# Kernel tuning notes

Hardware: AMD Instinct MI355X
Metric: run time of the kernel (lower is better)

The kernel has to match this reference:

```python
import math
import jax, jax.numpy as jnp
import numpy as np
from jax.scipy.linalg import cho_factor, cho_solve, block_diag

NUM_SENSORS = 64
T_STEPS = 2048
LOG2PI = float(np.log(2.0 * np.pi))

NCV_PROCESS_NOISE = np.array([[1.0/3.0, 0.0, 0.5, 0.0],
                              [0.0, 1.0/3.0, 0.0, 0.5],
                              [0.5, 0.0, 1.0, 0.0],
                              [0.0, 0.5, 0.0, 1.0]], dtype=np.float32)
NCV_TRANSITION_MATRIX = np.array([[1.0, 0.0, 1.0, 0.0],
                                  [0.0, 1.0, 0.0, 1.0],
                                  [0.0, 0.0, 1.0, 0.0],
                                  [0.0, 0.0, 0.0, 1.0]], dtype=np.float32)


def setup_inputs() -> dict:
    key = jax.random.key(0)
    k1, k2 = jax.random.split(key)
    track = jax.random.normal(k1, (T_STEPS, 2), dtype=jnp.float32)
    # positive covariance scales for the bias prior (torch param init ~ ones)
    bias_scales = jax.random.uniform(k2, (2,), jnp.float32, 0.5, 1.5)
    obs_noise = jnp.float32(0.7)
    trans_noise = jnp.float32(0.3)
    return {"track": track, "bias_scales": bias_scales,
            "obs_noise": obs_noise, "trans_noise": trans_noise}


def _hmm_forward(track, bias_scales, obs_noise, trans_noise, num_sensors):
    S = num_sensors
    OD = 2 * S           # obs_dim
    D = OD + 4           # augmented latent: [bias(OD); state(4)]
    T = track.shape[0]
    dt = track.dtype

    # observation matrix exactly as in torch source:
    # eye(4,2).expand(S,4,2).transpose(0,-1).reshape(4, OD)
    E = jnp.eye(4, 2, dtype=dt)
    Hobs = jnp.transpose(jnp.broadcast_to(E, (S, 4, 2)), (2, 1, 0)).reshape(4, OD)
    # augmented emission: y = bias + state @ Hobs  ->  H_aug z
    Haug = jnp.concatenate([jnp.eye(OD, dtype=dt), Hobs.T], axis=1)  # (OD, D)

    F = jnp.asarray(NCV_TRANSITION_MATRIX, dt)
    # trans scale_tril = trans_noise * chol(NCV_Q) -> cov = trans_noise^2 * NCV_Q
    Qs = (trans_noise ** 2) * jnp.asarray(NCV_PROCESS_NOISE, dt)
    A = block_diag(jnp.eye(OD, dtype=dt), F)                         # (D, D)
    Q = block_diag(jnp.zeros((OD, OD), dt), Qs)                      # (D, D)
    # obs scale_tril = obs_noise * I -> cov = obs_noise^2 * I
    R = (obs_noise ** 2) * jnp.eye(OD, dtype=dt)

    # bias prior covariance = diag(bias_scales interleaved per sensor)
    bias_var = jnp.broadcast_to(bias_scales, (S, 2)).reshape(-1)     # (OD,)
    m0 = jnp.zeros((D,), dt)
    P0 = jnp.diag(jnp.concatenate([bias_var, jnp.ones((4,), dt)]))

    # obs vector per step: x.expand(S,2).reshape(-1) (interleaved repeat)
    ys = jnp.broadcast_to(track[:, None, :], (T, S, 2)).reshape(T, OD)

    def step(carry, y):
        m, P, ll = carry
        # predict
        mp = A @ m
        Pp = A @ P @ A.T + Q
        # innovation
        HP = Haug @ Pp                      # (OD, D)
        Sm = HP @ Haug.T + R                # (OD, OD)
        cf = cho_factor(Sm, lower=True)
        v = y - Haug @ mp                   # (OD,)
        # update
        K = cho_solve(cf, HP)               # S^{-1} H Pp, (OD, D)
        m_new = mp + K.T @ v
        P_new = Pp - HP.T @ K
        P_new = 0.5 * (P_new + P_new.T)
        # log-likelihood of innovation
        logdet = 2.0 * jnp.sum(jnp.log(jnp.diag(cf[0])))
        quad = v @ cho_solve(cf, v)
        ll = ll - 0.5 * (OD * LOG2PI + logdet + quad)
        return (m_new, P_new, ll), None

    (mT, PT, ll), _ = jax.lax.scan(step, (m0, P0, jnp.zeros((), dt)), ys)
    # funsor's remaining Gaussian over (bias, state_T) has precision = inv(filtered cov)
    cfP = cho_factor(PT, lower=True)
    prec = cho_solve(cfP, jnp.eye(D, dtype=dt))
    return ll, prec


def reference(track, bias_scales, obs_noise, trans_noise):
    return _hmm_forward(track, bias_scales, obs_noise, trans_noise, NUM_SENSORS)
```

## Files before the change

### kernel.cpp

```cpp
#include <hip/hip_runtime.h>
#include <math.h>

#define L2PI 1.8378770664093454835606594728112
#define LN2  0.69314718055994530941723212145818

struct LP {
    float jFF, jFL, jFB, jLL, jLB, jBB;
    float hF, hL, hB, g, dm, de;
};

struct Cn { float qa, qb, qc, wa, wb, ri, Cstep; };

__device__ __forceinline__ float shf(float v, int s) { return __shfl(v, s, 64); }
__device__ __forceinline__ float sx (float v, int m) { return __shfl_xor(v, m, 64); }

#define LGKM0() do { \
    asm volatile("s_waitcnt lgkmcnt(0)" ::: "memory"); \
    __builtin_amdgcn_sched_barrier(0); \
} while (0)

#define OFF_S   0
#define OFF_F1  16
#define OFF_F2T 32
#define OFF_MT  48
#define OFF_HM  64
#define GSTRIDE 152

#define WSR_OFF 8192

__device__ __forceinline__ float4 ld4(const float* p) {
    return *(const float4*)p;
}
__device__ __forceinline__ float dot4(float4 a, float4 b) {
    float s = a.x * b.x;
    s = fmaf(a.y, b.y, s);
    s = fmaf(a.z, b.z, s);
    s = fmaf(a.w, b.w, s);
    return s;
}
__device__ __forceinline__ float sel4(float x0, float x1, float x2, float x3, int k) {
    return (k == 0) ? x0 : ((k == 1) ? x1 : ((k == 2) ? x2 : x3));
}

struct Adj4 { float e[4][4]; };
__device__ __forceinline__ Adj4 adj4(const float4& Ra, const float4& Rb,
                                     const float4& Rc, const float4& Rd) {
    float sS[4][4];
    sS[0][0]=Ra.x; sS[0][1]=Ra.y; sS[0][2]=Ra.z; sS[0][3]=Ra.w;
    sS[1][0]=Rb.x; sS[1][1]=Rb.y; sS[1][2]=Rb.z; sS[1][3]=Rb.w;
    sS[2][0]=Rc.x; sS[2][1]=Rc.y; sS[2][2]=Rc.z; sS[2][3]=Rc.w;
    sS[3][0]=Rd.x; sS[3][1]=Rd.y; sS[3][2]=Rd.z; sS[3][3]=Rd.w;
    Adj4 A;
    #pragma unroll
    for (int a = 0; a < 4; ++a) {
        const int c0 = (a == 0) ? 1 : 0;
        const int c1 = (a <= 1) ? 2 : 1;
        const int c2 = (a <= 2) ? 3 : 2;
        #pragma unroll
        for (int b = 0; b < 4; ++b) {
            const int r0 = (b == 0) ? 1 : 0;
            const int r1 = (b <= 1) ? 2 : 1;
            const int r2 = (b <= 2) ? 3 : 2;
            float m00 = sS[r0][c0], m01 = sS[r0][c1], m02 = sS[r0][c2];
            float m10 = sS[r1][c0], m11 = sS[r1][c1], m12 = sS[r1][c2];
            float m20 = sS[r2][c0], m21 = sS[r2][c1], m22 = sS[r2][c2];
            float d0 = fmaf(m11, m22, -m12*m21);
            float d1 = fmaf(m10, m22, -m12*m20);
            float d2 = fmaf(m10, m21, -m11*m20);
            float det3 = m00*d0 - m01*d1 + m02*d2;
            A.e[a][b] = (((a + b) & 1) ? -det3 : det3);
        }
    }
    return A;
}
__device__ __forceinline__ float det4_colj(const Adj4& A, const float4& RJ, int j) {
    float a0j = sel4(A.e[0][0], A.e[0][1], A.e[0][2], A.e[0][3], j);
    float a1j = sel4(A.e[1][0], A.e[1][1], A.e[1][2], A.e[1][3], j);
    float a2j = sel4(A.e[2][0], A.e[2][1], A.e[2][2], A.e[2][3], j);
    float a3j = sel4(A.e[3][0], A.e[3][1], A.e[3][2], A.e[3][3], j);
    float t0 = RJ.x * a0j, t1 = RJ.y * a1j, t2 = RJ.z * a2j, t3 = RJ.w * a3j;
    return (t0 + t1) + (t2 + t3);
}

__device__ __forceinline__ LP init_lane(float x0, float x1, const Cn& C, int i, int j) {
    LP P;
    float v = 0.0f;
    if (i == j) v = (i < 2) ? C.qa : C.qc;
    if ((i ^ j) == 2) v = C.wa;
    P.jFF = v;
    v = 0.0f;
    if (j == (i & 1))     v = (i < 2) ? -C.qa : -C.wa;
    if (j == (i & 1) + 2) v = (i < 2) ? -C.qb : -C.wb;
    P.jFL = v;
    P.jFB = 0.0f;
    v = 0.0f;
    if (i == j) v = ((i < 2) ? C.qa : C.qc) + (((i & 1) == 0) ? 2.0f*C.ri : 0.0f);
    if ((i ^ j) == 2) v = C.qb;
    P.jLL = v;
    P.jLB = (((i == 0) && (j < 2)) || ((i == 2) && (j >= 2))) ? C.ri : 0.0f;
    P.jBB = (i == j) ? C.ri : 0.0f;
    P.hF = 0.0f;
    P.hL = ((j & 1) == 0) ? C.ri * (x0 + x1) : 0.0f;
    P.hB = C.ri * ((j & 1) ? x1 : x0);
    P.g  = -C.ri * (x0*x0 + x1*x1) + C.Cstep;
    P.dm = 1.0f; P.de = 0.0f;
    return P;
}

__device__ __forceinline__ LP compose(const LP& P1, const LP& P2, float* gl, int i, int j) {
    float hm = P1.hL + P2.hF;
    float Mb = P1.jLB + P2.jFB;
    float S  = P1.jLL + P2.jFF;
    float dm = P1.dm * P2.dm;
    float de = P1.de + P2.de;
    { int ex; dm = frexpf(dm, &ex); de += (float)ex; }
    const int ij = 4*i + j, ji = 4*j + i;

    gl[OFF_S   + ij] = S;
    gl[OFF_F1  + ij] = P1.jFL;
    gl[OFF_F2T + ji] = P2.jFL;
    gl[OFF_MT  + ji] = Mb;
    if (i == 0) gl[OFF_HM + j] = hm;
    LGKM0();
    float4 Ra = ld4(gl + OFF_S + 0);
    float4 Rb = ld4(gl + OFF_S + 4);
    float4 Rc = ld4(gl + OFF_S + 8);
    float4 Rd = ld4(gl + OFF_S + 12);
    float4 RJ = ld4(gl + OFF_S + 4*j);
    float4 f1r4 = ld4(gl + OFF_F1  + 4*i);
    float4 f1T4 = ld4(gl + OFF_F1  + 4*j);
    float4 f2c4 = ld4(gl + OFF_F2T + 4*j);
    float4 f2T4 = ld4(gl + OFF_F2T + 4*i);
    float4 mc4  = ld4(gl + OFF_MT  + 4*j);
    float4 mT4  = ld4(gl + OFF_MT  + 4*i);
    float4 hm4  = ld4(gl + OFF_HM);

    Adj4 A = adj4(Ra, Rb, Rc, Rd);
    float det = det4_colj(A, RJ, j);
    dm *= det; { int ex; dm = frexpf(dm, &ex); de += (float)ex; }
    const float rdet = 1.0f / det;
    float4 sie0 = make_float4(A.e[0][0]*rdet, A.e[0][1]*rdet, A.e[0][2]*rdet, A.e[0][3]*rdet);
    float4 sie1 = make_float4(A.e[1][0]*rdet, A.e[1][1]*rdet, A.e[1][2]*rdet, A.e[1][3]*rdet);
    float4 sie2 = make_float4(A.e[2][0]*rdet, A.e[2][1]*rdet, A.e[2][2]*rdet, A.e[2][3]*rdet);
    float4 sie3 = make_float4(A.e[3][0]*rdet, A.e[3][1]*rdet, A.e[3][2]*rdet, A.e[3][3]*rdet);

    float4 a1r4 = make_float4(dot4(f1r4, sie0), dot4(f1r4, sie1),
                              dot4(f1r4, sie2), dot4(f1r4, sie3));
    float4 a1j4 = make_float4(dot4(f1T4, sie0), dot4(f1T4, sie1),
                              dot4(f1T4, sie2), dot4(f1T4, sie3));
    float4 c1c4 = make_float4(dot4(sie0, mc4), dot4(sie1, mc4),
                              dot4(sie2, mc4), dot4(sie3, mc4));
    float4 b2c4 = make_float4(dot4(sie0, f2c4), dot4(sie1, f2c4),
                              dot4(sie2, f2c4), dot4(sie3, f2c4));
    float4 v44  = make_float4(dot4(sie0, hm4), dot4(sie1, hm4),
                              dot4(sie2, hm4), dot4(sie3, hm4));

    LP R;
    R.jFF = P1.jFF - dot4(a1r4, f1T4);
    R.jFL = -dot4(a1r4, f2c4);
    R.jFB = P1.jFB - dot4(a1r4, mc4);
    R.jLL = P2.jLL - dot4(f2T4, b2c4);
    R.jLB = P2.jLB - dot4(f2T4, c1c4);
    R.jBB = P1.jBB + P2.jBB - dot4(mT4, c1c4);
    R.hF  = P1.hF - dot4(a1j4, hm4);
    R.hL  = P2.hL - dot4(f2c4, v44);
    R.hB  = P1.hB + P2.hB - dot4(mc4, v44);
    R.g   = P1.g + P2.g + 2.0f*(float)L2PI + 0.5f*dot4(hm4, v44);
    R.dm = dm; R.de = de;
    return R;
}

__device__ __forceinline__ LP fetchx(const LP& P, int m) {
    LP O;
    O.jFF = sx(P.jFF,m); O.jFL = sx(P.jFL,m); O.jFB = sx(P.jFB,m);
    O.jLL = sx(P.jLL,m); O.jLB = sx(P.jLB,m); O.jBB = sx(P.jBB,m);
    O.hF  = sx(P.hF,m);  O.hL  = sx(P.hL,m);  O.hB  = sx(P.hB,m);
    O.g   = sx(P.g,m);   O.dm  = sx(P.dm,m);  O.de  = sx(P.de,m);
    return O;
}
__device__ __forceinline__ LP csel(bool up, const LP& O, const LP& P) {
    LP A;
    A.jFF = up?O.jFF:P.jFF; A.jFL = up?O.jFL:P.jFL; A.jFB = up?O.jFB:P.jFB;
    A.jLL = up?O.jLL:P.jLL; A.jLB = up?O.jLB:P.jLB; A.jBB = up?O.jBB:P.jBB;
    A.hF  = up?O.hF :P.hF;  A.hL  = up?O.hL :P.hL;  A.hB  = up?O.hB :P.hB;
    A.g   = up?O.g  :P.g;   A.dm  = up?O.dm :P.dm;  A.de  = up?O.de :P.de;
    return A;
}
__device__ __forceinline__ void pot_store(float* p, const LP& P) {
    p[0]=P.jFF; p[1]=P.jFL; p[2]=P.jFB; p[3]=P.jLL; p[4]=P.jLB; p[5]=P.jBB;
    p[6]=P.hF;  p[7]=P.hL;  p[8]=P.hB;  p[9]=P.g;   p[10]=P.dm; p[11]=P.de;
}
__device__ __forceinline__ LP pot_load(const float* p) {
    LP P;
    P.jFF=p[0]; P.jFL=p[1]; P.jFB=p[2]; P.jLL=p[3]; P.jLB=p[4]; P.jBB=p[5];
    P.hF=p[6];  P.hL=p[7];  P.hB=p[8];  P.g=p[9];   P.dm=p[10]; P.de=p[11];
    return P;
}
__device__ __forceinline__ void pot_store4(float* p, const LP& P) {
    *(float4*)(p + 0) = make_float4(P.jFF, P.jFL, P.jFB, P.jLL);
    *(float4*)(p + 4) = make_float4(P.jLB, P.jBB, P.hF,  P.hL);
    *(float4*)(p + 8) = make_float4(P.hB,  P.g,   P.dm,  P.de);
}
__device__ __forceinline__ LP pot_load4(const float* p) {
    float4 a = ld4(p + 0), b = ld4(p + 4), c = ld4(p + 8);
    LP P;
    P.jFF=a.x; P.jFL=a.y; P.jFB=a.z; P.jLL=a.w;
    P.jLB=b.x; P.jBB=b.y; P.hF=b.z;  P.hL=b.w;
    P.hB=c.x;  P.g=c.y;   P.dm=c.z;  P.de=c.w;
    return P;
}

__global__ __launch_bounds__(512)
void hmm_produce(const float* __restrict__ track,
                 const float* __restrict__ obs_noise_p,
                 const float* __restrict__ trans_noise_p,
                 float* __restrict__ ws)
{
    __shared__ float pool[2][8][16][13];
    __shared__ __align__(16) float cbuf[32 * GSTRIDE];
    const int tid = (int)threadIdx.x;
    const int l = tid & 63, w = tid >> 6;
    const int i = (l >> 2) & 3, j = l & 3, g = (l >> 4) & 3;
    const int gid = w * 4 + g;
    float* gl = &cbuf[(size_t)gid * GSTRIDE];
    const int bid = (int)blockIdx.x;

    const double sg2d = (double)obs_noise_p[0] * (double)obs_noise_p[0];
    const double qn2d = (double)trans_noise_p[0] * (double)trans_noise_p[0];

    Cn C;
    C.qa = (float)(12.0/qn2d); C.qb = (float)(-6.0/qn2d); C.qc = (float)(4.0/qn2d);
    C.wa = (float)(6.0/qn2d);  C.wb = (float)(-2.0/qn2d);
    C.ri = (float)(32.0/sg2d);
    C.Cstep = (float)(-2.0*log(2.0*M_PI*sg2d/32.0) - 2.0*L2PI
                      - 0.5*(4.0*log(qn2d) - 2.0*log(12.0)));

    const int t0 = (bid * 32 + gid) * 2;
    LP P;
    #pragma unroll 1
    for (int op = 0; op < 6; ++op) {
        LP A, Bp;
        if (op == 0) {
            A  = init_lane(track[2*t0+0], track[2*t0+1], C, i, j);
            Bp = init_lane(track[2*t0+2], track[2*t0+3], C, i, j);
        } else if (op < 3) {
            const int m = 16 << (op - 1);
            LP O = fetchx(P, m);
            const bool up = (l & m) != 0;
            A  = csel(up, O, P);
            Bp = csel(up, P, O);
        } else {
            const int s = 1 << (op - 3);
            const int buf = (op - 3) & 1;
            if (l < 16) pot_store(&pool[buf][w][l][0], P);
            __syncthreads();
            LP O = pot_load(&pool[buf][w ^ s][l & 15][0]);
            const bool up = (w & s) != 0;
            A  = csel(up, O, P);
            Bp = csel(up, P, O);
        }
        P = compose(A, Bp, gl, i, j);
    }
    if (w == 0 && l < 16)
        pot_store4(ws + ((size_t)bid * 16 + l) * 12, P);
}

__global__ __launch_bounds__(512)
void hmm_tree(const float* __restrict__ bias_scales,
              const float* __restrict__ obs_noise_p,
              float* __restrict__ ws)
{
    __shared__ float pool[2][8][16][13];
    __shared__ __align__(16) float cbuf[32 * GSTRIDE];
    const int tid = (int)threadIdx.x;
    const int l = tid & 63, w = tid >> 6;
    const int i = (l >> 2) & 3, j = l & 3, g = (l >> 4) & 3;
    const int gid = w * 4 + g;
    float* gl = &cbuf[(size_t)gid * GSTRIDE];
    float* wsr = ws + WSR_OFF;

    const double sg2d = (double)obs_noise_p[0] * (double)obs_noise_p[0];
    const double a00 = (double)bias_scales[0];
    const double a01 = (double)bias_scales[1];
    const double Td = 2048.0;
    const double c0d = sg2d/a00, c1d = sg2d/a01;
    const double llconst = -31.0*(Td*(L2PI + log(sg2d)) + log((c0d+Td)/c0d))
                           -31.0*(Td*(L2PI + log(sg2d)) + log((c1d+Td)/c1d))
                           -2.0*Td*log(32.0);
    const float gconst = (float)(-4.0*L2PI + 2.0*log(32.0) - log(a00) - log(a01));

    LP P = pot_load4(ws + ((size_t)gid * 16 + (l & 15)) * 12);
    #pragma unroll 1
    for (int op = 0; op < 5; ++op) {
        LP A, Bp;
        if (op < 2) {
            const int m = 16 << op;
            LP O = fetchx(P, m);
            const bool up = (l & m) != 0;
            A  = csel(up, O, P);
            Bp = csel(up, P, O);
        } else {
            const int s = 1 << (op - 2);
            const int buf = (op - 2) & 1;
            if (l < 16) pot_store(&pool[buf][w][l][0], P);
            __syncthreads();
            LP O = pot_load(&pool[buf][w ^ s][l & 15][0]);
            const bool up = (w & s) != 0;
            A  = csel(up, O, P);
            Bp = csel(up, P, O);
        }
        P = compose(A, Bp, gl, i, j);
    }

    if (w == 0) {
        const float a0i = (float)((i & 1) ? a01 : a00);
        P.jFF += (i == j) ? 1.0f : 0.0f;
        P.jBB += (i == j) ? 32.0f / a0i : 0.0f;
        P.g   += gconst;
        float dm = P.dm, de = P.de;
        const int ij = 4*i + j, ji = 4*j + i;

        gl[OFF_S   + ij] = P.jFF;
        gl[OFF_F1  + ji] = P.jFL;
        gl[OFF_F2T + ji] = P.jFB;
        if (i == 0) gl[OFF_HM + j] = P.hF;
        LGKM0();
        float4 Ra = ld4(gl + OFF_S + 0);
        float4 Rb = ld4(gl + OFF_S + 4);
        float4 Rc = ld4(gl + OFF_S + 8);
        float4 Rd = ld4(gl + OFF_S + 12);
        float4 RJ = ld4(gl + OFF_S + 4*j);
        float4 fr4 = ld4(gl + OFF_F1  + 4*i);
        float4 fT4 = ld4(gl + OFF_F1  + 4*j);
        float4 bc4 = ld4(gl + OFF_F2T + 4*i);
        float4 bT4 = ld4(gl + OFF_F2T + 4*j);
        float4 hf4 = ld4(gl + OFF_HM);

        Adj4 A = adj4(Ra, Rb, Rc, Rd);
        float det = det4_colj(A, RJ, j);
        dm *= det; { int ex; dm = frexpf(dm, &ex); de += (float)ex; }
        const float rdet = 1.0f / det;
        float4 sie0 = make_float4(A.e[0][0]*rdet, A.e[0][1]*rdet, A.e[0][2]*rdet, A.e[0][3]*rdet);
        float4 sie1 = make_float4(A.e[1][0]*rdet, A.e[1][1]*rdet, A.e[1][2]*rdet, A.e[1][3]*rdet);
        float4 sie2 = make_float4(A.e[2][0]*rdet, A.e[2][1]*rdet, A.e[2][2]*rdet, A.e[2][3]*rdet);
        float4 sie3 = make_float4(A.e[3][0]*rdet, A.e[3][1]*rdet, A.e[3][2]*rdet, A.e[3][3]*rdet);

        float4 ylc4 = make_float4(dot4(sie0, fT4), dot4(sie1, fT4),
                                  dot4(sie2, fT4), dot4(sie3, fT4));
        float4 ybc4 = make_float4(dot4(sie0, bT4), dot4(sie1, bT4),
                                  dot4(sie2, bT4), dot4(sie3, bT4));
        float4 yfc4 = make_float4(dot4(sie0, hf4), dot4(sie1, hf4),
                                  dot4(sie2, hf4), dot4(sie3, hf4));
        float s1  = dot4(fr4, ylc4);
        float s2  = dot4(fr4, ybc4);
        float s3  = dot4(bc4, ybc4);
        float sh1 = dot4(fT4, yfc4);
        float sh2 = dot4(bT4, yfc4);
        float qF  = dot4(hf4, yfc4);

        float J8ss = P.jLL - s1;
        float J8sb = P.jLB - s2;
        float J8bb = P.jBB - s3;
        float h8s  = P.hL - sh1;
        float h8b  = P.hB - sh2;
        float g8   = P.g + 2.0f*(float)L2PI + 0.5f*qF;

        const int I = l >> 3, J = l & 7, i4 = I & 3, j4 = J & 3;
        float ss  = shf(J8ss, 4*i4 + j4);
        float sb  = shf(J8sb, 4*i4 + j4);
        float sbT = shf(J8sb, 4*j4 + i4);
        float bb  = shf(J8bb, 4*i4 + j4);
        float A8 = (I < 4) ? ((J < 4) ? ss : sb) : ((J < 4) ? sbT : bb);
        const float J8sav = A8;
        float h8v = (J < 4) ? shf(h8s, j4) : shf(h8b, j4);
        float h8r = (I < 4) ? shf(h8s, i4) : shf(h8b, i4);
        float K8 = (I == J) ? 1.0f : 0.0f;
        #pragma unroll 1
        for (int p = 0; p < 8; ++p) {
            float piv = shf(A8, 9*p);
            dm *= piv; { int ex; dm = frexpf(dm, &ex); de += (float)ex; }
            float ip = 1.0f / piv;
            float Ap = shf(A8, 8*p + J) * ip;
            float Kp = shf(K8, 8*p + J) * ip;
            float f  = shf(A8, 8*I + p);
            bool isp = (I == p);
            A8 = isp ? A8 * ip : fmaf(-f, Ap, A8);
            K8 = isp ? K8 * ip : fmaf(-f, Kp, K8);
        }
        float tq = h8r * K8 * h8v;
        tq += sx(tq,1); tq += sx(tq,2); tq += sx(tq,4);
        tq += sx(tq,8); tq += sx(tq,16); tq += sx(tq,32);

        double ll = (double)g8 + 4.0*L2PI
                    - 0.5*(log((double)dm) + (double)de*LN2) + 0.5*(double)tq;
        ll += llconst;

        const float i32 = 1.0f/32.0f, irn = 0.176776695296637f;
        int a = (I >= 4) ? I - 4 : I + 4;
        int b = (J >= 4) ? J - 4 : J + 4;
        float scale = (I >= 4 && J >= 4) ? i32 : (((I >= 4) != (J >= 4)) ? irn : 1.0f);
        wsr[1 + 8*a + b] = J8sav * scale;
        if (l < 4) {
            double a0k = (l & 1) ? a01 : a00;
            wsr[65 + l] = (float)(a0k*sg2d/(sg2d + Td*a0k));
        }
        if (l == 0) wsr[0] = (float)ll;
    }
}

__global__ __launch_bounds__(256)
void hmm_expand(const float* __restrict__ wsr,
                float* __restrict__ out)
{
    const int idx = (int)blockIdx.x * 256 + (int)threadIdx.x;
    const int total = 1 + 132*132;
    if (idx >= total) return;
    const float inv32 = 1.0f/32.0f;
    const float invrn = 0.176776695296637f;
    float v;
    if (idx == 0) {
        v = wsr[0];
    } else {
        int el = idx - 1;
        int r = el / 132;
        int cc = el - 132*r;
        if (r < 128) {
            int ki = ((r >> 6) << 1) | (r & 1);
            if (cc < 128) {
                int kj = ((cc >> 6) << 1) | (cc & 1);
                v = wsr[1 + 8*ki + kj] * inv32;
                if (ki == kj) {
                    float ia = 1.0f / wsr[65 + ki];
                    v -= ia * inv32;
                    if (r == cc) v += ia;
                }
            } else {
                v = wsr[1 + 8*ki + (cc - 124)] * invrn;
            }
        } else {
            if (cc < 128) {
                int kj = ((cc >> 6) << 1) | (cc & 1);
                v = wsr[1 + 8*kj + (r - 124)] * invrn;
            } else {
                v = wsr[1 + 8*(r - 124) + (cc - 124)];
            }
        }
    }
    out[idx] = v;
}

extern "C" void kernel_launch(void* const* d_in, const int* in_sizes, int n_in,
                              void* d_out, int out_size, void* d_ws, size_t ws_size,
                              hipStream_t stream) {
    (void)in_sizes; (void)n_in; (void)out_size; (void)ws_size;
    const float* track       = (const float*)d_in[0];
    const float* bias_scales = (const float*)d_in[1];
    const float* obs_noise   = (const float*)d_in[2];
    const float* trans_noise = (const float*)d_in[3];
    float* out = (float*)d_out;
    float* ws  = (float*)d_ws;
    hipLaunchKernelGGL(hmm_produce, dim3(32), dim3(512), 0, stream,
                       track, obs_noise, trans_noise, ws);
    hipLaunchKernelGGL(hmm_tree, dim3(1), dim3(512), 0, stream,
                       bias_scales, obs_noise, ws);
    hipLaunchKernelGGL(hmm_expand, dim3(69), dim3(256), 0, stream,
                       (const float*)(ws + WSR_OFF), out);
}
```

Measured before the change: 82.39 us.

## Distribute 4x4 inverse across lanes in tree compose and final reduction

In the tree kernel, the per-lane full adjugate/inverse of the 4x4 Schur block is replaced by each lane computing a single 3x3 cofactor, with the determinant reduced via xor shuffles. The inverse and the intermediate products are then exchanged through LDS (or, in the final step, through cross-lane shuffles) rather than every lane recomputing them redundantly. This reduces per-lane ALU work and register pressure but adds extra LDS round trips, waits and shuffles on a latency-bound serial path. The leaf kernel keeps the original compose.

New measurement: 81.36 us. About the same (-1.3%).

```diff
diff --git a/kernel.cpp b/kernel.cpp
--- a/kernel.cpp
+++ b/kernel.cpp
@@ -19,11 +19,21 @@
     __builtin_amdgcn_sched_barrier(0); \
 } while (0)
 
-#define OFF_S   0
-#define OFF_F1  16
-#define OFF_F2T 32
-#define OFF_MT  48
-#define OFF_HM  64
+#define PO_S   0
+#define PO_F1  16
+#define PO_F2T 32
+#define PO_MT  48
+#define PO_HM  64
+#define TO_S   0
+#define TO_SI  16
+#define TO_F1  32
+#define TO_F2T 48
+#define TO_MT  64
+#define TO_A1  80
+#define TO_C1T 96
+#define TO_B2T 112
+#define TO_V4  128
+#define TO_HM  132
 #define GSTRIDE 152
 
 #define WSR_OFF 8192
@@ -107,7 +117,7 @@
     return P;
 }
 
-__device__ __forceinline__ LP compose(const LP& P1, const LP& P2, float* gl, int i, int j) {
+__device__ __forceinline__ LP compose_li(const LP& P1, const LP& P2, float* gl, int i, int j) {
     float hm = P1.hL + P2.hF;
     float Mb = P1.jLB + P2.jFB;
     float S  = P1.jLL + P2.jFF;
@@ -116,24 +126,24 @@
     { int ex; dm = frexpf(dm, &ex); de += (float)ex; }
     const int ij = 4*i + j, ji = 4*j + i;
 
-    gl[OFF_S   + ij] = S;
-    gl[OFF_F1  + ij] = P1.jFL;
-    gl[OFF_F2T + ji] = P2.jFL;
-    gl[OFF_MT  + ji] = Mb;
-    if (i == 0) gl[OFF_HM + j] = hm;
+    gl[PO_S   + ij] = S;
+    gl[PO_F1  + ij] = P1.jFL;
+    gl[PO_F2T + ji] = P2.jFL;
+    gl[PO_MT  + ji] = Mb;
+    if (i == 0) gl[PO_HM + j] = hm;
     LGKM0();
-    float4 Ra = ld4(gl + OFF_S + 0);
-    float4 Rb = ld4(gl + OFF_S + 4);
-    float4 Rc = ld4(gl + OFF_S + 8);
-    float4 Rd = ld4(gl + OFF_S + 12);
-    float4 RJ = ld4(gl + OFF_S + 4*j);
-    float4 f1r4 = ld4(gl + OFF_F1  + 4*i);
-    float4 f1T4 = ld4(gl + OFF_F1  + 4*j);
-    float4 f2c4 = ld4(gl + OFF_F2T + 4*j);
-    float4 f2T4 = ld4(gl + OFF_F2T + 4*i);
-    float4 mc4  = ld4(gl + OFF_MT  + 4*j);
-    float4 mT4  = ld4(gl + OFF_MT  + 4*i);
-    float4 hm4  = ld4(gl + OFF_HM);
+    float4 Ra = ld4(gl + PO_S + 0);
+    float4 Rb = ld4(gl + PO_S + 4);
+    float4 Rc = ld4(gl + PO_S + 8);
+    float4 Rd = ld4(gl + PO_S + 12);
+    float4 RJ = ld4(gl + PO_S + 4*j);
+    float4 f1r4 = ld4(gl + PO_F1  + 4*i);
+    float4 f1T4 = ld4(gl + PO_F1  + 4*j);
+    float4 f2c4 = ld4(gl + PO_F2T + 4*j);
+    float4 f2T4 = ld4(gl + PO_F2T + 4*i);
+    float4 mc4  = ld4(gl + PO_MT  + 4*j);
+    float4 mT4  = ld4(gl + PO_MT  + 4*i);
+    float4 hm4  = ld4(gl + PO_HM);
 
     Adj4 A = adj4(Ra, Rb, Rc, Rd);
     float det = det4_colj(A, RJ, j);
@@ -154,6 +164,89 @@
                               dot4(sie2, f2c4), dot4(sie3, f2c4));
     float4 v44  = make_float4(dot4(sie0, hm4), dot4(sie1, hm4),
                               dot4(sie2, hm4), dot4(sie3, hm4));
+
+    LP R;
+    R.jFF = P1.jFF - dot4(a1r4, f1T4);
+    R.jFL = -dot4(a1r4, f2c4);
+    R.jFB = P1.jFB - dot4(a1r4, mc4);
+    R.jLL = P2.jLL - dot4(f2T4, b2c4);
+    R.jLB = P2.jLB - dot4(f2T4, c1c4);
+    R.jBB = P1.jBB + P2.jBB - dot4(mT4, c1c4);
+    R.hF  = P1.hF - dot4(a1j4, hm4);
+    R.hL  = P2.hL - dot4(f2c4, v44);
+    R.hB  = P1.hB + P2.hB - dot4(mc4, v44);
+    R.g   = P1.g + P2.g + 2.0f*(float)L2PI + 0.5f*dot4(hm4, v44);
+    R.dm = dm; R.de = de;
+    return R;
+}
+
+__device__ __forceinline__ LP compose_3r(const LP& P1, const LP& P2, float* gl, int i, int j) {
+    float hm = P1.hL + P2.hF;
+    float Mb = P1.jLB + P2.jFB;
+    float S  = P1.jLL + P2.jFF;
+    float dm = P1.dm * P2.dm;
+    float de = P1.de + P2.de;
+    { int ex; dm = frexpf(dm, &ex); de += (float)ex; }
+    const int ij = 4*i + j, ji = 4*j + i;
+
+    gl[TO_S   + ij] = S;
+    gl[TO_F1  + ij] = P1.jFL;
+    gl[TO_F2T + ji] = P2.jFL;
+    gl[TO_MT  + ji] = Mb;
+    if (i == 0) gl[TO_HM + j] = hm;
+    LGKM0();
+
+    const int r0 = (j == 0) ? 1 : 0;
+    const int r1 = (j <= 1) ? 2 : 1;
+    const int r2 = (j <= 2) ? 3 : 2;
+    float4 R0 = ld4(gl + TO_S + 4*r0);
+    float4 R1 = ld4(gl + TO_S + 4*r1);
+    float4 R2 = ld4(gl + TO_S + 4*r2);
+    float4 RJ = ld4(gl + TO_S + 4*j);
+    float4 f1r4 = ld4(gl + TO_F1  + 4*i);
+    float4 f1T4 = ld4(gl + TO_F1  + 4*j);
+    float4 f2c4 = ld4(gl + TO_F2T + 4*j);
+    float4 f2T4 = ld4(gl + TO_F2T + 4*i);
+    float4 mc4  = ld4(gl + TO_MT  + 4*j);
+    float4 mT4  = ld4(gl + TO_MT  + 4*i);
+    float4 hm4  = ld4(gl + TO_HM);
+
+    const bool i0 = (i == 0), i1 = (i <= 1), i2 = (i <= 2);
+    float m00 = i0 ? R0.y : R0.x, m01 = i1 ? R0.z : R0.y, m02 = i2 ? R0.w : R0.z;
+    float m10 = i0 ? R1.y : R1.x, m11 = i1 ? R1.z : R1.y, m12 = i2 ? R1.w : R1.z;
+    float m20 = i0 ? R2.y : R2.x, m21 = i1 ? R2.z : R2.y, m22 = i2 ? R2.w : R2.z;
+    float d0 = fmaf(m11, m22, -m12*m21);
+    float d1 = fmaf(m10, m22, -m12*m20);
+    float d2 = fmaf(m10, m21, -m11*m20);
+    float det3 = m00*d0 - m01*d1 + m02*d2;
+    float adj = (((i + j) & 1) ? -det3 : det3);
+    float sji = (i < 2) ? (i0 ? RJ.x : RJ.y) : ((i == 2) ? RJ.z : RJ.w);
+    float t = sji * adj;
+    t += sx(t, 4); t += sx(t, 8);
+    float det = t;
+    dm *= det; { int ex; dm = frexpf(dm, &ex); de += (float)ex; }
+    float Sio = adj * (1.0f / det);
+
+    gl[TO_SI + ij] = Sio;
+    LGKM0();
+    float4 sr4 = ld4(gl + TO_SI + 4*i);
+    float4 sc4 = ld4(gl + TO_SI + 4*j);
+
+    float A1  = dot4(f1r4, sc4);
+    float C1  = dot4(sr4,  mc4);
+    float B2  = dot4(sr4,  f2c4);
+    float v4i = dot4(sr4,  hm4);
+
+    gl[TO_A1  + ij] = A1;
+    gl[TO_C1T + ji] = C1;
+    gl[TO_B2T + ji] = B2;
+    if (i == j) gl[TO_V4 + i] = v4i;
+    LGKM0();
+    float4 a1r4 = ld4(gl + TO_A1  + 4*i);
+    float4 a1j4 = ld4(gl + TO_A1  + 4*j);
+    float4 c1c4 = ld4(gl + TO_C1T + 4*j);
+    float4 b2c4 = ld4(gl + TO_B2T + 4*j);
+    float4 v44  = ld4(gl + TO_V4);
 
     LP R;
     R.jFF = P1.jFF - dot4(a1r4, f1T4);
@@ -259,7 +352,7 @@
             A  = csel(up, O, P);
             Bp = csel(up, P, O);
         }
-        P = compose(A, Bp, gl, i, j);
+        P = compose_li(A, Bp, gl, i, j);
     }
     if (w == 0 && l < 16)
         pot_store4(ws + ((size_t)bid * 16 + l) * 12, P);
@@ -274,7 +367,7 @@
     __shared__ __align__(16) float cbuf[32 * GSTRIDE];
     const int tid = (int)threadIdx.x;
     const int l = tid & 63, w = tid >> 6;
-    const int i = (l >> 2) & 3, j = l & 3, g = (l >> 4) & 3;
+    const int i = (l >> 2) & 3, j = l & 3, gb = l & 48, g = (l >> 4) & 3;
     const int gid = w * 4 + g;
     float* gl = &cbuf[(size_t)gid * GSTRIDE];
     float* wsr = ws + WSR_OFF;
@@ -309,7 +402,7 @@
             A  = csel(up, O, P);
             Bp = csel(up, P, O);
         }
-        P = compose(A, Bp, gl, i, j);
+        P = compose_3r(A, Bp, gl, i, j);
     }
 
     if (w == 0) {
@@ -318,46 +411,61 @@
         P.jBB += (i == j) ? 32.0f / a0i : 0.0f;
         P.g   += gconst;
         float dm = P.dm, de = P.de;
-        const int ij = 4*i + j, ji = 4*j + i;
-
-        gl[OFF_S   + ij] = P.jFF;
-        gl[OFF_F1  + ji] = P.jFL;
-        gl[OFF_F2T + ji] = P.jFB;
-        if (i == 0) gl[OFF_HM + j] = P.hF;
-        LGKM0();
-        float4 Ra = ld4(gl + OFF_S + 0);
-        float4 Rb = ld4(gl + OFF_S + 4);
-        float4 Rc = ld4(gl + OFF_S + 8);
-        float4 Rd = ld4(gl + OFF_S + 12);
-        float4 RJ = ld4(gl + OFF_S + 4*j);
-        float4 fr4 = ld4(gl + OFF_F1  + 4*i);
-        float4 fT4 = ld4(gl + OFF_F1  + 4*j);
-        float4 bc4 = ld4(gl + OFF_F2T + 4*i);
-        float4 bT4 = ld4(gl + OFF_F2T + 4*j);
-        float4 hf4 = ld4(gl + OFF_HM);
-
-        Adj4 A = adj4(Ra, Rb, Rc, Rd);
-        float det = det4_colj(A, RJ, j);
+        float S = P.jFF;
+        const int r0 = (j == 0) ? 1 : 0;
+        const int r1 = (j <= 1) ? 2 : 1;
+        const int r2 = (j <= 2) ? 3 : 2;
+        const int c0 = (i == 0) ? 1 : 0;
+        const int c1 = (i <= 1) ? 2 : 1;
+        const int c2 = (i <= 2) ? 3 : 2;
+        float m00 = shf(S, gb + 4*r0 + c0), m01 = shf(S, gb + 4*r0 + c1), m02 = shf(S, gb + 4*r0 + c2);
+        float m10 = shf(S, gb + 4*r1 + c0), m11 = shf(S, gb + 4*r1 + c1), m12 = shf(S, gb + 4*r1 + c2);
+        float m20 = shf(S, gb + 4*r2 + c0), m21 = shf(S, gb + 4*r2 + c1), m22 = shf(S, gb + 4*r2 + c2);
+        float d0 = fmaf(m11, m22, -m12*m21);
+        float d1 = fmaf(m10, m22, -m12*m20);
+        float d2 = fmaf(m10, m21, -m11*m20);
+        float det3 = m00*d0 - m01*d1 + m02*d2;
+        float adj = (((i + j) & 1) ? -det3 : det3);
+        float sji = shf(S, gb + 4*j + i);
+        float tdet = sji * adj;
+        tdet += sx(tdet, 4); tdet += sx(tdet, 8);
+        float det = tdet;
         dm *= det; { int ex; dm = frexpf(dm, &ex); de += (float)ex; }
-        const float rdet = 1.0f / det;
-        float4 sie0 = make_float4(A.e[0][0]*rdet, A.e[0][1]*rdet, A.e[0][2]*rdet, A.e[0][3]*rdet);
-        float4 sie1 = make_float4(A.e[1][0]*rdet, A.e[1][1]*rdet, A.e[1][2]*rdet, A.e[1][3]*rdet);
-        float4 sie2 = make_float4(A.e[2][0]*rdet, A.e[2][1]*rdet, A.e[2][2]*rdet, A.e[2][3]*rdet);
-        float4 sie3 = make_float4(A.e[3][0]*rdet, A.e[3][1]*rdet, A.e[3][2]*rdet, A.e[3][3]*rdet);
-
-        float4 ylc4 = make_float4(dot4(sie0, fT4), dot4(sie1, fT4),
-                                  dot4(sie2, fT4), dot4(sie3, fT4));
-        float4 ybc4 = make_float4(dot4(sie0, bT4), dot4(sie1, bT4),
-                                  dot4(sie2, bT4), dot4(sie3, bT4));
-        float4 yfc4 = make_float4(dot4(sie0, hf4), dot4(sie1, hf4),
-                                  dot4(sie2, hf4), dot4(sie3, hf4));
-        float s1  = dot4(fr4, ylc4);
-        float s2  = dot4(fr4, ybc4);
-        float s3  = dot4(bc4, ybc4);
-        float sh1 = dot4(fT4, yfc4);
-        float sh2 = dot4(bT4, yfc4);
-        float qF  = dot4(hf4, yfc4);
-
+        const float Si = adj * (1.0f / det);
+        float sr[4], fr[4], fT[4], bc[4], bT[4], hfc[4];
+        #pragma unroll
+        for (int r = 0; r < 4; ++r) {
+            sr[r]  = shf(Si, gb + 4*i + r);
+            fr[r]  = shf(P.jFL, gb + 4*r + i);
+            fT[r]  = shf(P.jFL, gb + 4*r + j);
+            bc[r]  = shf(P.jFB, gb + 4*r + i);
+            bT[r]  = shf(P.jFB, gb + 4*r + j);
+            hfc[r] = shf(P.hF, gb + 5*r);
+        }
+        float YL = 0.0f, YB = 0.0f, yFi = 0.0f;
+        #pragma unroll
+        for (int r = 0; r < 4; ++r) {
+            YL  = fmaf(sr[r], fT[r], YL);
+            YB  = fmaf(sr[r], bT[r], YB);
+            yFi = fmaf(sr[r], hfc[r], yFi);
+        }
+        float ylc[4], ybc[4], yfc[4];
+        #pragma unroll
+        for (int r = 0; r < 4; ++r) {
+            ylc[r] = shf(YL, gb + 4*r + j);
+            ybc[r] = shf(YB, gb + 4*r + j);
+            yfc[r] = shf(yFi, gb + 5*r);
+        }
+        float s1 = 0.0f, s2 = 0.0f, s3 = 0.0f, sh1 = 0.0f, sh2 = 0.0f, qF = 0.0f;
+        #pragma unroll
+        for (int r = 0; r < 4; ++r) {
+            s1  = fmaf(fr[r], ylc[r], s1);
+            s2  = fmaf(fr[r], ybc[r], s2);
+            s3  = fmaf(bc[r], ybc[r], s3);
+            sh1 = fmaf(fT[r], yfc[r], sh1);
+            sh2 = fmaf(bT[r], yfc[r], sh2);
+            qF  = fmaf(hfc[r], yfc[r], qF);
+        }
         float J8ss = P.jLL - s1;
         float J8sb = P.jLB - s2;
         float J8bb = P.jBB - s3;
```
